# Kernel optimization log

Hardware: AMD Instinct MI355X
Metric: run time of the kernel (lower is better)

The kernel has to match this reference:

```python
import jax, jax.numpy as jnp
import numpy as np

POOL = 7
IMAGE_SHAPE = (1024, 1024, 3)


def _crop_and_resize(fmap, boxes, pool):
    """TF-style crop_and_resize with extrapolation_value=0.
    fmap: [C, H, W]; boxes: [N, (y1,x1,y2,x2)] normalized. Returns [N, C, pool, pool]."""
    C, H, W = fmap.shape
    dt = fmap.dtype
    y1, x1, y2, x2 = boxes[:, 0], boxes[:, 1], boxes[:, 2], boxes[:, 3]
    g = jnp.arange(pool, dtype=dt) / (pool - 1)  # [P] in [0,1]
    ys = (y1[:, None] + g[None, :] * (y2 - y1)[:, None]) * (H - 1)  # [N,P]
    xs = (x1[:, None] + g[None, :] * (x2 - x1)[:, None]) * (W - 1)  # [N,P]
    y0f = jnp.floor(ys); x0f = jnp.floor(xs)
    ly = (ys - y0f).astype(dt); lx = (xs - x0f).astype(dt)
    y0 = jnp.clip(y0f.astype(jnp.int32), 0, H - 1)
    y1i = jnp.clip(y0 + 1, 0, H - 1)
    x0 = jnp.clip(x0f.astype(jnp.int32), 0, W - 1)
    x1i = jnp.clip(x0 + 1, 0, W - 1)
    vy = ((ys >= 0) & (ys <= H - 1)).astype(dt)  # extrapolation_value = 0 outside
    vx = ((xs >= 0) & (xs <= W - 1)).astype(dt)

    def at(yi, xi):
        # gather -> [C, N, P, P]
        return fmap[:, yi[:, :, None], xi[:, None, :]]

    wy0 = (1 - ly)[None, :, :, None]; wy1 = ly[None, :, :, None]
    wx0 = (1 - lx)[None, :, None, :]; wx1 = lx[None, :, None, :]
    val = (at(y0, x0) * wy0 + at(y1i, x0) * wy1) * wx0 \
        + (at(y0, x1i) * wy0 + at(y1i, x1i) * wy1) * wx1
    val = val * (vy[None, :, :, None] * vx[None, :, None, :])
    return jnp.transpose(val, (1, 0, 2, 3))  # [N, C, P, P]


def reference(boxes, p2, p3, p4, p5):
    """pyramid_roi_align: route each box to FPN level 2..5 via the 224-scale
    log2 heuristic, then CropAndResize(pool, pool, 0) from that level.
    Output order matches input box order (original sorts back by box_to_level)."""
    h = boxes[:, 2] - boxes[:, 0]
    w = boxes[:, 3] - boxes[:, 1]
    image_area = float(IMAGE_SHAPE[0] * IMAGE_SHAPE[1])
    roi_level = 4.0 + jnp.log2(jnp.sqrt(h * w) / (224.0 / np.sqrt(image_area)))
    roi_level = jnp.clip(jnp.round(roi_level).astype(jnp.int32), 2, 5)
    boxes_d = jax.lax.stop_gradient(boxes)  # level_boxes.detach() in original
    fmaps = [p2, p3, p4, p5]
    pooled = jnp.zeros((boxes.shape[0], p2.shape[0], POOL, POOL), dtype=p2.dtype)
    for i, level in enumerate(range(2, 6)):
        mask = (roi_level == level).astype(p2.dtype)[:, None, None, None]
        pooled = pooled + mask * _crop_and_resize(fmaps[i], boxes_d, POOL)
    return pooled


def setup_inputs():
    key = jax.random.key(0)
    kb, ks, k2, k3, k4, k5 = jax.random.split(key, 6)
    N, C = 1000, 256
    size = jax.random.uniform(ks, (N, 2), minval=0.02, maxval=0.9)
    tl = jax.random.uniform(kb, (N, 2)) * (1.0 - size)  # top-left so box stays in [0,1]
    boxes = jnp.concatenate([tl[:, 0:1], tl[:, 1:2],
                             tl[:, 0:1] + size[:, 0:1], tl[:, 1:2] + size[:, 1:2]], axis=1)
    p2 = jax.random.normal(k2, (C, 256, 256), jnp.float32)
    p3 = jax.random.normal(k3, (C, 128, 128), jnp.float32)
    p4 = jax.random.normal(k4, (C, 64, 64), jnp.float32)
    p5 = jax.random.normal(k5, (C, 32, 32), jnp.float32)
    return {"boxes": boxes, "p2": p2, "p3": p3, "p4": p4, "p5": p5}
```

## Files before the change

### kernel.cpp

```cpp
#include <hip/hip_runtime.h>


#define POOL 7
#define NCH  256
#define ELEMS_PER_BOX (NCH * POOL * POOL)
#define CHUNKS 7
#define CHUNK_ELEMS (ELEMS_PER_BOX / CHUNKS)

__global__ __launch_bounds__(256) void roi_align_kernel(
    const float* __restrict__ boxes,
    const float* __restrict__ p2, const float* __restrict__ p3,
    const float* __restrict__ p4, const float* __restrict__ p5,
    float* __restrict__ out, int N)
{
    const int bid   = blockIdx.x;
    const int n     = bid % N;
    const int chunk = bid / N;

    __shared__ int   s_y0[POOL], s_y1[POOL], s_x0[POOL], s_x1[POOL];
    __shared__ float s_ly[POOL], s_lx[POOL], s_vy[POOL], s_vx[POOL];
    __shared__ int   s_H;
    __shared__ const float* s_fmap;

    const int tid = threadIdx.x;

    if (tid < 2 * POOL) {
        const float by1 = boxes[4 * n + 0];
        const float bx1 = boxes[4 * n + 1];
        const float by2 = boxes[4 * n + 2];
        const float bx2 = boxes[4 * n + 3];
        const float h = by2 - by1;
        const float w = bx2 - bx1;
        float rl = 4.0f + log2f(sqrtf(h * w) / 0.21875f);
        int level = (int)rintf(rl);
        level = min(5, max(2, level));
        const int H = 256 >> (level - 2);
        if (tid == 0) {
            s_H = H;
            s_fmap = (level == 2) ? p2 : (level == 3) ? p3 : (level == 4) ? p4 : p5;
        }
        const bool isx = (tid >= POOL);
        const int  g   = isx ? tid - POOL : tid;
        const float c1 = isx ? bx1 : by1;
        const float c2 = isx ? bx2 : by2;
        const float t  = (float)g / (float)(POOL - 1);
        const float s  = (c1 + t * (c2 - c1)) * (float)(H - 1);
        const float f0 = floorf(s);
        const float l  = s - f0;
        int i0 = (int)f0;
        i0 = min(H - 1, max(0, i0));
        const int i1 = min(H - 1, i0 + 1);
        const float v = (s >= 0.0f && s <= (float)(H - 1)) ? 1.0f : 0.0f;
        if (isx) { s_x0[g] = i0; s_x1[g] = i1; s_lx[g] = l; s_vx[g] = v; }
        else     { s_y0[g] = i0; s_y1[g] = i1; s_ly[g] = l; s_vy[g] = v; }
    }
    __syncthreads();

    const float* __restrict__ fmap = s_fmap;
    const int H = s_H;
    const int W = H;
    float* __restrict__ obase = out + (size_t)n * ELEMS_PER_BOX + chunk * CHUNK_ELEMS;
    const int ibase = chunk * CHUNK_ELEMS + tid;

    float v00[CHUNKS], v10[CHUNKS], v01[CHUNKS], v11[CHUNKS];
    float wgt[CHUNKS][4];
    float vv[CHUNKS];

#pragma unroll
    for (int k = 0; k < CHUNKS; ++k) {
        const int i  = ibase + k * 256;
        const int c  = i / 49;
        const int pp = i - c * 49;
        const int py = pp / 7;
        const int px = pp - py * 7;

        const float* __restrict__ f = fmap + (size_t)c * (H * W);
        const int y0 = s_y0[py], y1 = s_y1[py];
        const int x0 = s_x0[px], x1 = s_x1[px];

        v00[k] = f[y0 * W + x0];
        v10[k] = f[y1 * W + x0];
        v01[k] = f[y0 * W + x1];
        v11[k] = f[y1 * W + x1];

        const float ly = s_ly[py], lx = s_lx[px];
        wgt[k][0] = (1.0f - ly) * (1.0f - lx);
        wgt[k][1] = ly * (1.0f - lx);
        wgt[k][2] = (1.0f - ly) * lx;
        wgt[k][3] = ly * lx;
        vv[k] = s_vy[py] * s_vx[px];
    }

#pragma unroll
    for (int k = 0; k < CHUNKS; ++k) {
        float val = v00[k] * wgt[k][0] + v10[k] * wgt[k][1]
                  + v01[k] * wgt[k][2] + v11[k] * wgt[k][3];
        obase[tid + k * 256] = val * vv[k];
    }
}

extern "C" void kernel_launch(void* const* d_in, const int* in_sizes, int n_in,
                              void* d_out, int out_size, void* d_ws, size_t ws_size,
                              hipStream_t stream) {
    const float* boxes = (const float*)d_in[0];
    const float* p2    = (const float*)d_in[1];
    const float* p3    = (const float*)d_in[2];
    const float* p4    = (const float*)d_in[3];
    const float* p5    = (const float*)d_in[4];
    float* out = (float*)d_out;
    const int N = in_sizes[0] / 4;

    roi_align_kernel<<<N * CHUNKS, 256, 0, stream>>>(boxes, p2, p3, p4, p5, out, N);
}
```

Measured before the change: 154.1 us.

## Precompute per-cell offsets and weights, fetch horizontal neighbor pairs as float2

Setup now runs on 49 threads, one per output cell. Each builds combined row offsets and folded bilinear and validity weights for its cell. The two horizontal neighbors x0 and x0+1 are read with one 8-byte vector load; when x0 is at the last column the load shifts one left and the weights are adjusted. The per-element divisions by 49 and 7 are replaced by incremental channel/cell stepping, and the weight products are loaded from shared memory. This halves global load instructions and trims integer work in a gather-bound kernel, but the vector loads may hit 4-byte-aligned-only addresses.

```diff
diff --git a/kernel.cpp b/kernel.cpp
--- a/kernel.cpp
+++ b/kernel.cpp
@@ -6,6 +6,8 @@
 #define ELEMS_PER_BOX (NCH * POOL * POOL)
 #define CHUNKS 7
 #define CHUNK_ELEMS (ELEMS_PER_BOX / CHUNKS)
+
+typedef float f2 __attribute__((ext_vector_type(2)));
 
 __global__ __launch_bounds__(256) void roi_align_kernel(
     const float* __restrict__ boxes,
@@ -17,14 +19,15 @@
     const int n     = bid % N;
     const int chunk = bid / N;
 
-    __shared__ int   s_y0[POOL], s_y1[POOL], s_x0[POOL], s_x1[POOL];
-    __shared__ float s_ly[POOL], s_lx[POOL], s_vy[POOL], s_vx[POOL];
-    __shared__ int   s_H;
+    __shared__ int   s_off0[49], s_off1[49];
+    __shared__ float s_a[49], s_b[49];
+    __shared__ float s_w0[49], s_w1[49];
+    __shared__ int   s_HW;
     __shared__ const float* s_fmap;
 
     const int tid = threadIdx.x;
 
-    if (tid < 2 * POOL) {
+    if (tid < 49) {
         const float by1 = boxes[4 * n + 0];
         const float bx1 = boxes[4 * n + 1];
         const float by2 = boxes[4 * n + 2];
@@ -35,67 +38,73 @@
         int level = (int)rintf(rl);
         level = min(5, max(2, level));
         const int H = 256 >> (level - 2);
+        const int W = H;
         if (tid == 0) {
-            s_H = H;
+            s_HW = H * W;
             s_fmap = (level == 2) ? p2 : (level == 3) ? p3 : (level == 4) ? p4 : p5;
         }
-        const bool isx = (tid >= POOL);
-        const int  g   = isx ? tid - POOL : tid;
-        const float c1 = isx ? bx1 : by1;
-        const float c2 = isx ? bx2 : by2;
-        const float t  = (float)g / (float)(POOL - 1);
-        const float s  = (c1 + t * (c2 - c1)) * (float)(H - 1);
-        const float f0 = floorf(s);
-        const float l  = s - f0;
-        int i0 = (int)f0;
-        i0 = min(H - 1, max(0, i0));
-        const int i1 = min(H - 1, i0 + 1);
-        const float v = (s >= 0.0f && s <= (float)(H - 1)) ? 1.0f : 0.0f;
-        if (isx) { s_x0[g] = i0; s_x1[g] = i1; s_lx[g] = l; s_vx[g] = v; }
-        else     { s_y0[g] = i0; s_y1[g] = i1; s_ly[g] = l; s_vy[g] = v; }
+        const int py = tid / 7;
+        const int px = tid - 7 * py;
+
+        const float ty = (float)py / (float)(POOL - 1);
+        const float ys = (by1 + ty * (by2 - by1)) * (float)(H - 1);
+        const float yf = floorf(ys);
+        const float ly = ys - yf;
+        int y0 = (int)yf; y0 = min(H - 1, max(0, y0));
+        const int y1 = min(H - 1, y0 + 1);
+        const float vy = (ys >= 0.0f && ys <= (float)(H - 1)) ? 1.0f : 0.0f;
+
+        const float tx = (float)px / (float)(POOL - 1);
+        const float xs = (bx1 + tx * (bx2 - bx1)) * (float)(W - 1);
+        const float xf = floorf(xs);
+        const float lx = xs - xf;
+        int x0 = (int)xf; x0 = min(W - 1, max(0, x0));
+        const float vx = (xs >= 0.0f && xs <= (float)(W - 1)) ? 1.0f : 0.0f;
+
+        const int xb = min(x0, W - 2);
+        const bool edge = (x0 != xb);
+        const float a = edge ? 0.0f : vx * (1.0f - lx);
+        const float b = edge ? vx : vx * lx;
+
+        s_off0[tid] = y0 * W + xb;
+        s_off1[tid] = y1 * W + xb;
+        s_a[tid] = a;
+        s_b[tid] = b;
+        s_w0[tid] = vy * (1.0f - ly);
+        s_w1[tid] = vy * ly;
     }
     __syncthreads();
 
     const float* __restrict__ fmap = s_fmap;
-    const int H = s_H;
-    const int W = H;
+    const int HW = s_HW;
+
+    const int i0 = chunk * CHUNK_ELEMS + tid;
+    int c  = i0 / 49;
+    int pp = i0 - c * 49;
+
+    f2  q0[CHUNKS], q1[CHUNKS];
+    int cell[CHUNKS];
+    {
+        int cc = c, p = pp;
+#pragma unroll
+        for (int k = 0; k < CHUNKS; ++k) {
+            cell[k] = p;
+            const float* plane = fmap + (size_t)cc * HW;
+            q0[k] = *(const f2*)(plane + s_off0[p]);
+            q1[k] = *(const f2*)(plane + s_off1[p]);
+            cc += 5; p += 11;
+            if (p >= 49) { p -= 49; cc += 1; }
+        }
+    }
+
     float* __restrict__ obase = out + (size_t)n * ELEMS_PER_BOX + chunk * CHUNK_ELEMS;
-    const int ibase = chunk * CHUNK_ELEMS + tid;
-
-    float v00[CHUNKS], v10[CHUNKS], v01[CHUNKS], v11[CHUNKS];
-    float wgt[CHUNKS][4];
-    float vv[CHUNKS];
-
 #pragma unroll
     for (int k = 0; k < CHUNKS; ++k) {
-        const int i  = ibase + k * 256;
-        const int c  = i / 49;
-        const int pp = i - c * 49;
-        const int py = pp / 7;
-        const int px = pp - py * 7;
-
-        const float* __restrict__ f = fmap + (size_t)c * (H * W);
-        const int y0 = s_y0[py], y1 = s_y1[py];
-        const int x0 = s_x0[px], x1 = s_x1[px];
-
-        v00[k] = f[y0 * W + x0];
-        v10[k] = f[y1 * W + x0];
-        v01[k] = f[y0 * W + x1];
-        v11[k] = f[y1 * W + x1];
-
-        const float ly = s_ly[py], lx = s_lx[px];
-        wgt[k][0] = (1.0f - ly) * (1.0f - lx);
-        wgt[k][1] = ly * (1.0f - lx);
-        wgt[k][2] = (1.0f - ly) * lx;
-        wgt[k][3] = ly * lx;
-        vv[k] = s_vy[py] * s_vx[px];
-    }
-
-#pragma unroll
-    for (int k = 0; k < CHUNKS; ++k) {
-        float val = v00[k] * wgt[k][0] + v10[k] * wgt[k][1]
-                  + v01[k] * wgt[k][2] + v11[k] * wgt[k][3];
-        obase[tid + k * 256] = val * vv[k];
+        const int p = cell[k];
+        const float a = s_a[p], b = s_b[p];
+        const float r0 = q0[k].x * a + q0[k].y * b;
+        const float r1 = q1[k].x * a + q1[k].y * b;
+        obase[tid + k * 256] = r0 * s_w0[p] + r1 * s_w1[p];
     }
 }
 
```

New measurement: 142.8 us. 1.08x faster.
